# Performance work log

Hardware: AMD Instinct MI355X
Metric: run time of the kernel (lower is better)

## Reference

```python
import jax, jax.numpy as jnp
import numpy as np

B, S, D, DK, DV = 8, 2048, 256, 128, 128

def setup_inputs() -> dict:
    key = jax.random.key(0)
    ks = jax.random.split(key, 9)
    return {
        "x_q": jax.random.normal(ks[0], (B, S, D), jnp.float32),
        "x_k": jax.random.normal(ks[1], (B, S, D), jnp.float32),
        "x_v": jax.random.normal(ks[2], (B, S, D), jnp.float32),
        "Wq": jax.random.normal(ks[3], (D, DK), jnp.float32) * (1.0 / np.sqrt(D)),
        "bq": jax.random.normal(ks[4], (DK,), jnp.float32) * 0.02,
        "Wk": jax.random.normal(ks[5], (D, DK), jnp.float32) * (1.0 / np.sqrt(D)),
        "bk": jax.random.normal(ks[6], (DK,), jnp.float32) * 0.02,
        "Wv": jax.random.normal(ks[7], (D, DV), jnp.float32) * (1.0 / np.sqrt(D)),
        "bv": jax.random.normal(ks[8], (DV,), jnp.float32) * 0.02,
    }

def reference(x_q, x_k, x_v, Wq, bq, Wk, bk, Wv, bv):
    # Dense projections: [B,S,D] @ [D,dk] + bias
    q = jnp.einsum("bsd,dk->bsk", x_q, Wq) + bq
    k = jnp.einsum("bsd,dk->bsk", x_k, Wk) + bk
    v = jnp.einsum("bsd,dv->bsv", x_v, Wv) + bv
    scale = 1.0 / np.sqrt(Wq.shape[1]).astype(np.float32)  # 1/sqrt(d_k)
    scores = jnp.einsum("bqk,bsk->bqs", q, k) * scale       # [B,S,S]
    attn = jax.nn.softmax(scores, axis=-1)
    return jnp.einsum("bqs,bsv->bqv", attn, v)               # [B,S,d_v]
```

## Files before the change

kernel.cpp:

```cpp
#include <hip/hip_runtime.h>
#include <stdint.h>

typedef float    f32x4 __attribute__((ext_vector_type(4)));
typedef _Float16 f16x8 __attribute__((ext_vector_type(8)));
typedef _Float16 f16x4 __attribute__((ext_vector_type(4)));
typedef unsigned int u32x4 __attribute__((ext_vector_type(4)));

#define SPLIT 4

__device__ __forceinline__ f32x4 mfma16(f16x8 a, f16x8 b, f32x4 c) {
    return __builtin_amdgcn_mfma_f32_16x16x32_f16(a, b, c, 0, 0, 0);
}

__global__ __launch_bounds__(256) void prep_weights(
    const float* __restrict__ Wq, const float* __restrict__ Wk,
    const float* __restrict__ Wv, _Float16* __restrict__ wt) {
    __shared__ float Ls[64 * 65];
    const int bx = blockIdx.x;
    const int w  = bx >> 3, t = bx & 7;
    const int k0 = (t >> 1) * 64, n0 = (t & 1) * 64;
    const float* W = (w == 0) ? Wq : (w == 1) ? Wk : Wv;
    const int tid = threadIdx.x;
    #pragma unroll
    for (int i = 0; i < 16; i++) {
        int idx = i * 256 + tid;
        int r = idx >> 6, c = idx & 63;
        Ls[r * 65 + c] = W[(k0 + r) * 128 + n0 + c];
    }
    __syncthreads();
    #pragma unroll
    for (int i = 0; i < 16; i++) {
        int idx = i * 256 + tid;
        int r2 = idx >> 6, c2 = idx & 63;
        wt[w * 32768 + (n0 + r2) * 256 + k0 + c2] = (_Float16)Ls[c2 * 65 + r2];
    }
}

__global__ __launch_bounds__(256) void proj_kernel(
    const float* __restrict__ xq, const float* __restrict__ xk,
    const float* __restrict__ xv, const _Float16* __restrict__ wt,
    const float* __restrict__ bq, const float* __restrict__ bk,
    const float* __restrict__ bv,
    _Float16* __restrict__ qo, _Float16* __restrict__ ko,
    _Float16* __restrict__ vtmp)
{
    const int mode = blockIdx.y;
    const float*    X    = mode == 0 ? xq : mode == 1 ? xk : xv;
    const float*    bias = mode == 0 ? bq : mode == 1 ? bk : bv;
    const _Float16* W    = wt + mode * 32768;
    _Float16*       Y    = mode == 0 ? qo : mode == 1 ? ko : vtmp;

    const int tid  = threadIdx.x;
    const int wave = tid >> 6, lane = tid & 63;
    const int ln   = lane & 15, qd = lane >> 4;
    const int row0 = blockIdx.x * 64 + wave * 16;

    const float*    xrow = X + (size_t)(row0 + ln) * 256 + qd * 8;
    const _Float16* wb   = W + ln * 256 + qd * 8;

    f32x4 acc[8];
    #pragma unroll
    for (int i = 0; i < 8; i++) acc[i] = (f32x4){0.f, 0.f, 0.f, 0.f};

    #pragma unroll
    for (int kk = 0; kk < 8; kk++) {
        f32x4 a0 = *(const f32x4*)(xrow + kk * 32);
        f32x4 a1 = *(const f32x4*)(xrow + kk * 32 + 4);
        f16x8 af;
        af[0] = (_Float16)a0[0]; af[1] = (_Float16)a0[1];
        af[2] = (_Float16)a0[2]; af[3] = (_Float16)a0[3];
        af[4] = (_Float16)a1[0]; af[5] = (_Float16)a1[1];
        af[6] = (_Float16)a1[2]; af[7] = (_Float16)a1[3];
        #pragma unroll
        for (int nt = 0; nt < 8; nt++) {
            f16x8 bf = *(const f16x8*)(wb + nt * 4096 + kk * 32);
            acc[nt] = mfma16(af, bf, acc[nt]);
        }
    }

    const float SC = 0.08838834764831845f * 1.4426950408889634f;
    #pragma unroll
    for (int nt = 0; nt < 8; nt++) {
        int col = nt * 16 + ln;
        float bb = bias[col];
        #pragma unroll
        for (int r = 0; r < 4; r++) {
            int orow = row0 + qd * 4 + r;
            float val = acc[nt][r] + bb;
            if (mode == 0) val *= SC;
            Y[(size_t)orow * 128 + col] = (_Float16)val;
        }
    }
}

__global__ __launch_bounds__(256) void transpose_v(
    const _Float16* __restrict__ vtmp, _Float16* __restrict__ vt)
{
    __shared__ __align__(16) _Float16 Ls[64 * 72];
    const int b  = blockIdx.z;
    const int s0 = blockIdx.x * 64;
    const int d0 = blockIdx.y * 64;
    const int tid = threadIdx.x;
    #pragma unroll
    for (int i = 0; i < 2; i++) {
        int idx = i * 256 + tid;
        int r = idx >> 3, c = (idx & 7) * 8;
        *(f16x8*)&Ls[r * 72 + c] =
            *(const f16x8*)(vtmp + (size_t)(b * 2048 + s0 + r) * 128 + d0 + c);
    }
    __syncthreads();
    #pragma unroll
    for (int i = 0; i < 2; i++) {
        int idx = i * 256 + tid;
        int dr = idx >> 3, sc8 = (idx & 7) * 8;
        f16x8 o;
        #pragma unroll
        for (int j = 0; j < 8; j++) o[j] = Ls[(sc8 + j) * 72 + dr];
        *(f16x8*)(vt + (size_t)(b * 128 + d0 + dr) * 2048 + s0 + sc8) = o;
    }
}

__global__ __launch_bounds__(512, 4) void attn_kernel(
    const _Float16* __restrict__ qp, const _Float16* __restrict__ kp,
    const _Float16* __restrict__ vtp, _Float16* __restrict__ opart,
    float2* __restrict__ ml)
{
    const int b  = blockIdx.y;
    const int z  = blockIdx.z;
    const int q0 = blockIdx.x * 128;
    const int tid  = threadIdx.x;
    const int wave = tid >> 6, lane = tid & 63;
    const int ln   = lane & 15, qd = lane >> 4;

    __shared__ __align__(16) _Float16 Ks[64 * 136];
    __shared__ __align__(16) _Float16 Vs[128 * 72];
    __shared__ __align__(16) _Float16 Ps[8 * 16 * 72];

    const _Float16* qrow =
        qp + (size_t)(b * 2048 + q0 + wave * 16 + ln) * 128 + qd * 8;
    f16x8 qf[4];
    #pragma unroll
    for (int c = 0; c < 4; c++) qf[c] = *(const f16x8*)(qrow + c * 32);

    f32x4 o[8];
    #pragma unroll
    for (int i = 0; i < 8; i++) o[i] = (f32x4){0.f, 0.f, 0.f, 0.f};
    float m_run[4] = {-1e30f, -1e30f, -1e30f, -1e30f};
    float l_run[4] = {0.f, 0.f, 0.f, 0.f};

    const _Float16* kbase = kp + (size_t)b * 2048 * 128;
    const _Float16* vbase = vtp + (size_t)b * 128 * 2048;

    for (int kt = z * 8; kt < z * 8 + 8; kt++) {
        __syncthreads();
        const _Float16* ks = kbase + kt * 64 * 128;
        #pragma unroll
        for (int i = tid; i < 1024; i += 512) {
            int r = i >> 4, c = i & 15;
            *(u32x4*)&Ks[r * 136 + c * 8] = *(const u32x4*)(ks + r * 128 + c * 8);
        }
        const _Float16* vs = vbase + kt * 64;
        #pragma unroll
        for (int i = tid; i < 1024; i += 512) {
            int r = i >> 3, c = i & 7;
            *(u32x4*)&Vs[r * 72 + c * 8] =
                *(const u32x4*)(vs + (size_t)r * 2048 + c * 8);
        }
        __syncthreads();

        f32x4 sc[4];
        #pragma unroll
        for (int st = 0; st < 4; st++) {
            sc[st] = (f32x4){0.f, 0.f, 0.f, 0.f};
            int base = (st * 16 + ln) * 136 + qd * 8;
            #pragma unroll
            for (int c = 0; c < 4; c++) {
                f16x8 kf = *(const f16x8*)&Ks[base + c * 32];
                sc[st] = mfma16(qf[c], kf, sc[st]);
            }
        }

        float mnew[4], alpha[4];
        #pragma unroll
        for (int r = 0; r < 4; r++) {
            float t = fmaxf(fmaxf(sc[0][r], sc[1][r]), fmaxf(sc[2][r], sc[3][r]));
            t = fmaxf(t, __shfl_xor(t, 1));
            t = fmaxf(t, __shfl_xor(t, 2));
            t = fmaxf(t, __shfl_xor(t, 4));
            t = fmaxf(t, __shfl_xor(t, 8));
            mnew[r]  = fmaxf(m_run[r], t);
            alpha[r] = exp2f(m_run[r] - mnew[r]);
        }
        #pragma unroll
        for (int st = 0; st < 4; st++)
            #pragma unroll
            for (int r = 0; r < 4; r++) {
                float p = exp2f(sc[st][r] - mnew[r]);
                sc[st][r] = p;
                Ps[wave * 1152 + (qd * 4 + r) * 72 + st * 16 + ln] = (_Float16)p;
            }
        #pragma unroll
        for (int r = 0; r < 4; r++) {
            float s = sc[0][r] + sc[1][r] + sc[2][r] + sc[3][r];
            s += __shfl_xor(s, 1); s += __shfl_xor(s, 2);
            s += __shfl_xor(s, 4); s += __shfl_xor(s, 8);
            l_run[r] = l_run[r] * alpha[r] + s;
            m_run[r] = mnew[r];
        }
        #pragma unroll
        for (int dt = 0; dt < 8; dt++)
            #pragma unroll
            for (int r = 0; r < 4; r++) o[dt][r] *= alpha[r];

        #pragma unroll
        for (int c = 0; c < 2; c++) {
            f16x8 pf = *(const f16x8*)&Ps[wave * 1152 + ln * 72 + c * 32 + qd * 8];
            #pragma unroll
            for (int dt = 0; dt < 8; dt++) {
                f16x8 vf = *(const f16x8*)&Vs[(dt * 16 + ln) * 72 + c * 32 + qd * 8];
                o[dt] = mfma16(pf, vf, o[dt]);
            }
        }
    }

    const size_t prow = (size_t)(z * 8 + b) * 2048 + q0 + wave * 16;
    _Float16* op = opart + (prow + qd * 4) * 128;
    #pragma unroll
    for (int dt = 0; dt < 8; dt++)
        #pragma unroll
        for (int r = 0; r < 4; r++)
            op[(size_t)r * 128 + dt * 16 + ln] = (_Float16)o[dt][r];
    if (ln == 0) {
        #pragma unroll
        for (int r = 0; r < 4; r++) {
            float2 v; v.x = m_run[r]; v.y = l_run[r];
            ml[prow + qd * 4 + r] = v;
        }
    }
}

__global__ __launch_bounds__(256) void merge_kernel(
    const _Float16* __restrict__ opart, const float2* __restrict__ ml,
    float* __restrict__ out)
{
    const int t = threadIdx.x;
    const int r = t >> 4, cg = t & 15;
    const size_t row = (size_t)blockIdx.x * 16 + r;

    float m[SPLIT], l[SPLIT], w[SPLIT];
    float M = -1e30f;
    #pragma unroll
    for (int zi = 0; zi < SPLIT; zi++) {
        float2 p = ml[(size_t)zi * 16384 + row];
        m[zi] = p.x; l[zi] = p.y; M = fmaxf(M, p.x);
    }
    float L = 0.f;
    #pragma unroll
    for (int zi = 0; zi < SPLIT; zi++) { w[zi] = exp2f(m[zi] - M); L += w[zi] * l[zi]; }
    const float inv = 1.0f / L;

    float acc[8] = {0.f, 0.f, 0.f, 0.f, 0.f, 0.f, 0.f, 0.f};
    #pragma unroll
    for (int zi = 0; zi < SPLIT; zi++) {
        f16x8 v = *(const f16x8*)&opart[((size_t)zi * 16384 + row) * 128 + cg * 8];
        #pragma unroll
        for (int j = 0; j < 8; j++) acc[j] += w[zi] * (float)v[j];
    }
    float* op = out + row * 128 + cg * 8;
    f32x4 lo = (f32x4){acc[0] * inv, acc[1] * inv, acc[2] * inv, acc[3] * inv};
    f32x4 hi = (f32x4){acc[4] * inv, acc[5] * inv, acc[6] * inv, acc[7] * inv};
    *(f32x4*)op = lo;
    *(f32x4*)(op + 4) = hi;
}

extern "C" void kernel_launch(void* const* d_in, const int* in_sizes, int n_in,
                              void* d_out, int out_size, void* d_ws, size_t ws_size,
                              hipStream_t stream) {
    const float* xq = (const float*)d_in[0];
    const float* xk = (const float*)d_in[1];
    const float* xv = (const float*)d_in[2];
    const float* Wq = (const float*)d_in[3];
    const float* bq = (const float*)d_in[4];
    const float* Wk = (const float*)d_in[5];
    const float* bk = (const float*)d_in[6];
    const float* Wv = (const float*)d_in[7];
    const float* bv = (const float*)d_in[8];
    float* out = (float*)d_out;

    char* ws = (char*)d_ws;
    _Float16* wt    = (_Float16*)ws;
    _Float16* qo    = (_Float16*)(ws + 196608);
    _Float16* ko    = (_Float16*)(ws + 196608 + 4194304);
    _Float16* vt    = (_Float16*)(ws + 196608 + 2 * 4194304);
    _Float16* opart = (_Float16*)(ws + 196608 + 3 * 4194304);
    _Float16* vtmp  = opart;
    float2*   ml    = (float2*)  (ws + 196608 + 3 * 4194304 + 16777216);

    hipLaunchKernelGGL(prep_weights, dim3(24), dim3(256), 0, stream,
                       Wq, Wk, Wv, wt);
    hipLaunchKernelGGL(proj_kernel, dim3(256, 3), dim3(256), 0, stream,
                       xq, xk, xv, wt, bq, bk, bv, qo, ko, vtmp);
    hipLaunchKernelGGL(transpose_v, dim3(32, 2, 8), dim3(256), 0, stream,
                       vtmp, vt);
    hipLaunchKernelGGL(attn_kernel, dim3(16, 8, SPLIT), dim3(512), 0, stream,
                       qo, ko, vt, opart, ml);
    hipLaunchKernelGGL(merge_kernel, dim3(1024), dim3(256), 0, stream,
                       opart, ml, out);
}
```

Measured before the change: 175.3 us.

## Keep P in registers via transposed MFMA, drop LDS staging, raise split

Computes S^T by swapping MFMA operands so each lane holds one query column. The softmax probabilities can then feed a 16x16x16 MFMA directly from registers, with no round-trip through the per-wave LDS P buffer. Row max and sum reductions now need only two cross-lane shuffles per wave. The split-K factor becomes runtime and rises to 8 when the workspace allows, and the launch bound changes to six blocks per SM. The risk is more partial output traffic in the merge and smaller-K MFMAs for the PV product.

```diff
diff --git a/kernel.cpp b/kernel.cpp
--- a/kernel.cpp
+++ b/kernel.cpp
@@ -6,10 +6,11 @@
 typedef _Float16 f16x4 __attribute__((ext_vector_type(4)));
 typedef unsigned int u32x4 __attribute__((ext_vector_type(4)));
 
-#define SPLIT 4
-
 __device__ __forceinline__ f32x4 mfma16(f16x8 a, f16x8 b, f32x4 c) {
     return __builtin_amdgcn_mfma_f32_16x16x32_f16(a, b, c, 0, 0, 0);
+}
+__device__ __forceinline__ f32x4 mfma16k16(f16x4 a, f16x4 b, f32x4 c) {
+    return __builtin_amdgcn_mfma_f32_16x16x16f16(a, b, c, 0, 0, 0);
 }
 
 __global__ __launch_bounds__(256) void prep_weights(
@@ -120,10 +121,10 @@
     }
 }
 
-__global__ __launch_bounds__(512, 4) void attn_kernel(
+__global__ __launch_bounds__(512, 6) void attn_kernel(
     const _Float16* __restrict__ qp, const _Float16* __restrict__ kp,
     const _Float16* __restrict__ vtp, _Float16* __restrict__ opart,
-    float2* __restrict__ ml)
+    float2* __restrict__ ml, int ntiles)
 {
     const int b  = blockIdx.y;
     const int z  = blockIdx.z;
@@ -134,7 +135,6 @@
 
     __shared__ __align__(16) _Float16 Ks[64 * 136];
     __shared__ __align__(16) _Float16 Vs[128 * 72];
-    __shared__ __align__(16) _Float16 Ps[8 * 16 * 72];
 
     const _Float16* qrow =
         qp + (size_t)(b * 2048 + q0 + wave * 16 + ln) * 128 + qd * 8;
@@ -145,13 +145,12 @@
     f32x4 o[8];
     #pragma unroll
     for (int i = 0; i < 8; i++) o[i] = (f32x4){0.f, 0.f, 0.f, 0.f};
-    float m_run[4] = {-1e30f, -1e30f, -1e30f, -1e30f};
-    float l_run[4] = {0.f, 0.f, 0.f, 0.f};
+    float m_run = -1e30f, l_run = 0.f;
 
     const _Float16* kbase = kp + (size_t)b * 2048 * 128;
     const _Float16* vbase = vtp + (size_t)b * 128 * 2048;
 
-    for (int kt = z * 8; kt < z * 8 + 8; kt++) {
+    for (int kt = z * ntiles; kt < z * ntiles + ntiles; kt++) {
         __syncthreads();
         const _Float16* ks = kbase + kt * 64 * 128;
         #pragma unroll
@@ -176,96 +175,87 @@
             #pragma unroll
             for (int c = 0; c < 4; c++) {
                 f16x8 kf = *(const f16x8*)&Ks[base + c * 32];
-                sc[st] = mfma16(qf[c], kf, sc[st]);
+                sc[st] = mfma16(kf, qf[c], sc[st]);
             }
         }
 
-        float mnew[4], alpha[4];
-        #pragma unroll
-        for (int r = 0; r < 4; r++) {
-            float t = fmaxf(fmaxf(sc[0][r], sc[1][r]), fmaxf(sc[2][r], sc[3][r]));
-            t = fmaxf(t, __shfl_xor(t, 1));
-            t = fmaxf(t, __shfl_xor(t, 2));
-            t = fmaxf(t, __shfl_xor(t, 4));
-            t = fmaxf(t, __shfl_xor(t, 8));
-            mnew[r]  = fmaxf(m_run[r], t);
-            alpha[r] = exp2f(m_run[r] - mnew[r]);
-        }
+        float t = sc[0][0];
         #pragma unroll
         for (int st = 0; st < 4; st++)
             #pragma unroll
+            for (int r = 0; r < 4; r++) t = fmaxf(t, sc[st][r]);
+        t = fmaxf(t, __shfl_xor(t, 16));
+        t = fmaxf(t, __shfl_xor(t, 32));
+        const float mnew  = fmaxf(m_run, t);
+        const float alpha = exp2f(m_run - mnew);
+
+        f16x4 ph[4];
+        float ssum = 0.f;
+        #pragma unroll
+        for (int st = 0; st < 4; st++) {
+            #pragma unroll
             for (int r = 0; r < 4; r++) {
-                float p = exp2f(sc[st][r] - mnew[r]);
-                sc[st][r] = p;
-                Ps[wave * 1152 + (qd * 4 + r) * 72 + st * 16 + ln] = (_Float16)p;
+                float p = exp2f(sc[st][r] - mnew);
+                ssum += p;
+                ph[st][r] = (_Float16)p;
             }
-        #pragma unroll
-        for (int r = 0; r < 4; r++) {
-            float s = sc[0][r] + sc[1][r] + sc[2][r] + sc[3][r];
-            s += __shfl_xor(s, 1); s += __shfl_xor(s, 2);
-            s += __shfl_xor(s, 4); s += __shfl_xor(s, 8);
-            l_run[r] = l_run[r] * alpha[r] + s;
-            m_run[r] = mnew[r];
-        }
+        }
+        ssum += __shfl_xor(ssum, 16);
+        ssum += __shfl_xor(ssum, 32);
+        l_run = l_run * alpha + ssum;
+        m_run = mnew;
+
         #pragma unroll
         for (int dt = 0; dt < 8; dt++)
             #pragma unroll
-            for (int r = 0; r < 4; r++) o[dt][r] *= alpha[r];
-
-        #pragma unroll
-        for (int c = 0; c < 2; c++) {
-            f16x8 pf = *(const f16x8*)&Ps[wave * 1152 + ln * 72 + c * 32 + qd * 8];
+            for (int r = 0; r < 4; r++) o[dt][r] *= alpha;
+
+        #pragma unroll
+        for (int st = 0; st < 4; st++) {
             #pragma unroll
             for (int dt = 0; dt < 8; dt++) {
-                f16x8 vf = *(const f16x8*)&Vs[(dt * 16 + ln) * 72 + c * 32 + qd * 8];
-                o[dt] = mfma16(pf, vf, o[dt]);
+                f16x4 vf = *(const f16x4*)&Vs[(dt * 16 + ln) * 72 + st * 16 + qd * 4];
+                o[dt] = mfma16k16(vf, ph[st], o[dt]);
             }
         }
     }
 
     const size_t prow = (size_t)(z * 8 + b) * 2048 + q0 + wave * 16;
-    _Float16* op = opart + (prow + qd * 4) * 128;
-    #pragma unroll
-    for (int dt = 0; dt < 8; dt++)
-        #pragma unroll
-        for (int r = 0; r < 4; r++)
-            op[(size_t)r * 128 + dt * 16 + ln] = (_Float16)o[dt][r];
-    if (ln == 0) {
-        #pragma unroll
-        for (int r = 0; r < 4; r++) {
-            float2 v; v.x = m_run[r]; v.y = l_run[r];
-            ml[prow + qd * 4 + r] = v;
-        }
+    _Float16* op = opart + (prow + ln) * 128 + qd * 4;
+    #pragma unroll
+    for (int dt = 0; dt < 8; dt++) {
+        f16x4 h;
+        #pragma unroll
+        for (int r = 0; r < 4; r++) h[r] = (_Float16)o[dt][r];
+        *(f16x4*)(op + dt * 16) = h;
+    }
+    if (qd == 0) {
+        float2 v; v.x = m_run; v.y = l_run;
+        ml[prow + ln] = v;
     }
 }
 
 __global__ __launch_bounds__(256) void merge_kernel(
     const _Float16* __restrict__ opart, const float2* __restrict__ ml,
-    float* __restrict__ out)
+    float* __restrict__ out, int split)
 {
     const int t = threadIdx.x;
     const int r = t >> 4, cg = t & 15;
     const size_t row = (size_t)blockIdx.x * 16 + r;
 
-    float m[SPLIT], l[SPLIT], w[SPLIT];
     float M = -1e30f;
-    #pragma unroll
-    for (int zi = 0; zi < SPLIT; zi++) {
+    for (int zi = 0; zi < split; zi++) M = fmaxf(M, ml[(size_t)zi * 16384 + row].x);
+    float L = 0.f;
+    float acc[8] = {0.f, 0.f, 0.f, 0.f, 0.f, 0.f, 0.f, 0.f};
+    for (int zi = 0; zi < split; zi++) {
         float2 p = ml[(size_t)zi * 16384 + row];
-        m[zi] = p.x; l[zi] = p.y; M = fmaxf(M, p.x);
-    }
-    float L = 0.f;
-    #pragma unroll
-    for (int zi = 0; zi < SPLIT; zi++) { w[zi] = exp2f(m[zi] - M); L += w[zi] * l[zi]; }
+        float w = exp2f(p.x - M);
+        L += w * p.y;
+        f16x8 v = *(const f16x8*)&opart[((size_t)zi * 16384 + row) * 128 + cg * 8];
+        #pragma unroll
+        for (int j = 0; j < 8; j++) acc[j] += w * (float)v[j];
+    }
     const float inv = 1.0f / L;
-
-    float acc[8] = {0.f, 0.f, 0.f, 0.f, 0.f, 0.f, 0.f, 0.f};
-    #pragma unroll
-    for (int zi = 0; zi < SPLIT; zi++) {
-        f16x8 v = *(const f16x8*)&opart[((size_t)zi * 16384 + row) * 128 + cg * 8];
-        #pragma unroll
-        for (int j = 0; j < 8; j++) acc[j] += w[zi] * (float)v[j];
-    }
     float* op = out + row * 128 + cg * 8;
     f32x4 lo = (f32x4){acc[0] * inv, acc[1] * inv, acc[2] * inv, acc[3] * inv};
     f32x4 hi = (f32x4){acc[4] * inv, acc[5] * inv, acc[6] * inv, acc[7] * inv};
@@ -292,9 +282,13 @@
     _Float16* qo    = (_Float16*)(ws + 196608);
     _Float16* ko    = (_Float16*)(ws + 196608 + 4194304);
     _Float16* vt    = (_Float16*)(ws + 196608 + 2 * 4194304);
-    _Float16* opart = (_Float16*)(ws + 196608 + 3 * 4194304);
+    float2*   ml    = (float2*)  (ws + 196608 + 3 * 4194304);
+    _Float16* opart = (_Float16*)(ws + 196608 + 3 * 4194304 + 1048576);
     _Float16* vtmp  = opart;
-    float2*   ml    = (float2*)  (ws + 196608 + 3 * 4194304 + 16777216);
+
+    const size_t base = 196608 + 3 * 4194304 + 1048576;
+    const int split = (ws_size >= base + (size_t)8 * 4194304) ? 8 : 4;
+    const int ntiles = 32 / split;
 
     hipLaunchKernelGGL(prep_weights, dim3(24), dim3(256), 0, stream,
                        Wq, Wk, Wv, wt);
@@ -302,8 +296,8 @@
                        xq, xk, xv, wt, bq, bk, bv, qo, ko, vtmp);
     hipLaunchKernelGGL(transpose_v, dim3(32, 2, 8), dim3(256), 0, stream,
                        vtmp, vt);
-    hipLaunchKernelGGL(attn_kernel, dim3(16, 8, SPLIT), dim3(512), 0, stream,
-                       qo, ko, vt, opart, ml);
+    hipLaunchKernelGGL(attn_kernel, dim3(16, 8, split), dim3(512), 0, stream,
+                       qo, ko, vt, opart, ml, ntiles);
     hipLaunchKernelGGL(merge_kernel, dim3(1024), dim3(256), 0, stream,
-                       opart, ml, out);
-}
+                       opart, ml, out, split);
+}
```

New measurement: 223.8 us. 1.28x slower.
